# Kernel optimization log

Measured on AMD Instinct MI355X. Metric: run time of the kernel, lower is better.

The kernel has to match this reference:

```python
import jax, jax.numpy as jnp
import numpy as np

K = 3  # hardcoded in TransitionUp.forward

def setup_inputs() -> dict:
    key = jax.random.key(0)
    ks = jax.random.split(key, 8)
    M, N = 32768, 8192
    UP_C, DOWN_C, OUT_C = 128, 256, 128
    return {
        "up_points": jax.random.normal(ks[0], (M, 3), dtype=jnp.float32),
        "up_features": jax.random.normal(ks[1], (M, UP_C), dtype=jnp.float32),
        "down_points": jax.random.normal(ks[2], (N, 3), dtype=jnp.float32),
        "down_features": jax.random.normal(ks[3], (N, DOWN_C), dtype=jnp.float32),
        # torch nn.Linear params: W [out,in], b [out]
        "W_up": jax.random.normal(ks[4], (OUT_C, UP_C), dtype=jnp.float32) / np.sqrt(UP_C),
        "b_up": jax.random.normal(ks[5], (OUT_C,), dtype=jnp.float32) * 0.01,
        "W_down": jax.random.normal(ks[6], (OUT_C, DOWN_C), dtype=jnp.float32) / np.sqrt(DOWN_C),
        "b_down": jax.random.normal(ks[7], (OUT_C,), dtype=jnp.float32) * 0.01,
    }

def interpolate_knn(query_points, dataset_points, dataset_features, k):
    # squared pairwise distances [M, N]
    delta = query_points[:, None, :] - dataset_points[None, :, :]
    dist = jnp.sum(delta * delta, axis=-1)
    neg_dist, knn_idx = jax.lax.top_k(-dist, k)  # smallest-k
    knn_dist = -neg_dist                           # [M, k]
    knn_feats = dataset_features[knn_idx]          # [M, k, C]
    recip = 1.0 / (knn_dist + 1e-8)
    weights = recip / jnp.sum(recip, axis=-1, keepdims=True)  # [M, k]
    return jnp.einsum('mk,mkc->mc', weights, knn_feats)

def reference(up_points, up_features, down_points, down_features, W_up, b_up, W_down, b_down):
    down_f = down_features @ W_down.T + b_down            # [N, OUT_C]
    interp_f = interpolate_knn(up_points, down_points, down_f, K)  # [M, OUT_C]
    return interp_f + (up_features @ W_up.T + b_up)
```

## Files before the change

### kernel.cpp

```cpp
#include <hip/hip_runtime.h>
#include <cfloat>

#define M_UP   32768
#define N_DOWN 8192
#define UPC    128
#define DOWNC  256
#define OUTC   128
#define NCHUNK 8
#define CHUNK  (N_DOWN / NCHUNK)
#define G      8
#define Q      2
#define PG     12

__device__ __forceinline__ void fma4(float4& acc, float s, const float4 w) {
    acc.x = fmaf(s, w.x, acc.x);
    acc.y = fmaf(s, w.y, acc.y);
    acc.z = fmaf(s, w.z, acc.z);
    acc.w = fmaf(s, w.w, acc.w);
}

__device__ __forceinline__ void top3_bl(float s, int idx,
                                        float& d0, float& d1, float& d2,
                                        int& i0, int& i1, int& i2) {
    bool c0 = s < d0, c1 = s < d1, c2 = s < d2;
    float n0 = fminf(d0, s);
    float n1 = __builtin_amdgcn_fmed3f(d0, d1, s);
    float n2 = __builtin_amdgcn_fmed3f(d1, d2, s);
    int m0 = c0 ? idx : i0;
    int m1 = c0 ? i0 : (c1 ? idx : i1);
    int m2 = c1 ? i1 : (c2 ? idx : i2);
    d0 = n0; d1 = n1; d2 = n2;
    i0 = m0; i1 = m1; i2 = m2;
}

__global__ __launch_bounds__(256) void transpose_w(
        const float* __restrict__ W_up, const float* __restrict__ W_down,
        float* __restrict__ wt_up, float* __restrict__ wt_down) {
    int e = blockIdx.x * 256 + threadIdx.x;
    if (e < DOWNC * OUTC) {
        int k = e >> 7, c = e & 127;
        wt_down[e] = W_down[c * DOWNC + k];
    } else {
        int e2 = e - DOWNC * OUTC;
        int k = e2 >> 7, c = e2 & 127;
        wt_up[e2] = W_up[c * UPC + k];
    }
}

template <int K>
__device__ __forceinline__ void gemm_tile32(
        const float* __restrict__ A, const float* __restrict__ WT,
        float* sA , float* sW ,
        int rbase, int tid, float4 acc[2][2]) {
    const int rl = tid & 15;
    const int c0 = (tid >> 4) * 8;
    #pragma unroll 1
    for (int ph = 0; ph < K / 32; ++ph) {
        if (ph) __syncthreads();
        {
            int r = tid >> 3, k4 = tid & 7;
            float4 v = *(const float4*)(A + (size_t)(rbase + r) * K + ph * 32 + k4 * 4);
            *(float4*)&sA[r * 36 + k4 * 4] = v;
        }
        #pragma unroll
        for (int i = 0; i < 4; ++i) {
            int idx = tid + i * 256;
            int kk = idx >> 5, cc = idx & 31;
            float4 v = *(const float4*)(WT + (size_t)(ph * 32 + kk) * OUTC + cc * 4);
            *(float4*)&sW[kk * OUTC + cc * 4] = v;
        }
        __syncthreads();
        #pragma unroll 4
        for (int kk = 0; kk < 32; ++kk) {
            float a0 = sA[rl * 36 + kk];
            float a1 = sA[(rl + 16) * 36 + kk];
            float4 w0 = *(const float4*)&sW[kk * OUTC + c0];
            float4 w1 = *(const float4*)&sW[kk * OUTC + c0 + 4];
            fma4(acc[0][0], a0, w0); fma4(acc[0][1], a0, w1);
            fma4(acc[1][0], a1, w0); fma4(acc[1][1], a1, w1);
        }
    }
}

__device__ __forceinline__ void down_body(
        const float* __restrict__ A, const float* __restrict__ WT,
        const float* __restrict__ bias, float* __restrict__ down_f,
        int rb, int tid, float* smem) {
    float* sA = smem;
    float* sW = smem + 1152;
    float4 acc[2][2] = {};
    gemm_tile32<DOWNC>(A, WT, sA, sW, rb * 32, tid, acc);
    const int rl = tid & 15;
    const int cg = (tid >> 4) * 2;
    const float4 b0 = ((const float4*)bias)[cg];
    const float4 b1 = ((const float4*)bias)[cg + 1];
    #pragma unroll
    for (int i = 0; i < 2; ++i) {
        const int row = rb * 32 + rl + 16 * i;
        float4 v0 = acc[i][0], v1 = acc[i][1];
        v0.x += b0.x; v0.y += b0.y; v0.z += b0.z; v0.w += b0.w;
        v1.x += b1.x; v1.y += b1.y; v1.z += b1.z; v1.w += b1.w;
        ((float4*)down_f)[row * 32 + cg] = v0;
        ((float4*)down_f)[row * 32 + cg + 1] = v1;
    }
}

__device__ __forceinline__ void knn_body(
        const float* __restrict__ up_points,
        const float* __restrict__ down_points,
        float2* __restrict__ part,
        int bx, int by, int tid, float* smem) {
    float* sx = smem;
    float* sy = smem + 1536;
    float* sz = smem + 3072;
    const int base = by * CHUNK;
    for (int t = tid; t < CHUNK; t += 256) {
        int g = base + t;
        int gi = t >> 3, j = t & 7;
        sx[PG * gi + j] = down_points[3 * g];
        sy[PG * gi + j] = down_points[3 * g + 1];
        sz[PG * gi + j] = down_points[3 * g + 2];
    }
    __syncthreads();

    const int m0 = bx * (256 * Q) + tid;
    const int m1 = m0 + 256;
    const float q0x = up_points[3 * m0];
    const float q0y = up_points[3 * m0 + 1];
    const float q0z = up_points[3 * m0 + 2];
    const float q1x = up_points[3 * m1];
    const float q1y = up_points[3 * m1 + 1];
    const float q1z = up_points[3 * m1 + 2];

    float a_gd0 = FLT_MAX, a_gd1 = FLT_MAX, a_gd2 = FLT_MAX;
    int   a_gi0 = 0, a_gi1 = 0, a_gi2 = 0;
    float b_gd0 = FLT_MAX, b_gd1 = FLT_MAX, b_gd2 = FLT_MAX;
    int   b_gi0 = 0, b_gi1 = 0, b_gi2 = 0;

    for (int gi = 0; gi < CHUNK / G; ++gi) {
        float4 x0 = *(const float4*)&sx[PG * gi], x1 = *(const float4*)&sx[PG * gi + 4];
        float4 y0 = *(const float4*)&sy[PG * gi], y1 = *(const float4*)&sy[PG * gi + 4];
        float4 z0 = *(const float4*)&sz[PG * gi], z1 = *(const float4*)&sz[PG * gi + 4];
        float px[G] = {x0.x, x0.y, x0.z, x0.w, x1.x, x1.y, x1.z, x1.w};
        float py[G] = {y0.x, y0.y, y0.z, y0.w, y1.x, y1.y, y1.z, y1.w};
        float pz[G] = {z0.x, z0.y, z0.z, z0.w, z1.x, z1.y, z1.z, z1.w};
        float s0[G], s1[G];
        #pragma unroll
        for (int j = 0; j < G; ++j) {
            float dx0 = q0x - px[j], dy0 = q0y - py[j], dz0 = q0z - pz[j];
            s0[j] = fmaf(dz0, dz0, fmaf(dy0, dy0, dx0 * dx0));
            float dx1 = q1x - px[j], dy1 = q1y - py[j], dz1 = q1z - pz[j];
            s1[j] = fmaf(dz1, dz1, fmaf(dy1, dy1, dx1 * dx1));
        }
        float gm0 = fminf(fminf(fminf(s0[0], s0[1]), fminf(s0[2], s0[3])),
                          fminf(fminf(s0[4], s0[5]), fminf(s0[6], s0[7])));
        float gm1 = fminf(fminf(fminf(s1[0], s1[1]), fminf(s1[2], s1[3])),
                          fminf(fminf(s1[4], s1[5]), fminf(s1[6], s1[7])));
        top3_bl(gm0, gi, a_gd0, a_gd1, a_gd2, a_gi0, a_gi1, a_gi2);
        top3_bl(gm1, gi, b_gd0, b_gd1, b_gd2, b_gi0, b_gi1, b_gi2);
    }

    #pragma unroll
    for (int qq = 0; qq < Q; ++qq) {
        const float qx = qq ? q1x : q0x;
        const float qy = qq ? q1y : q0y;
        const float qz = qq ? q1z : q0z;
        int bases[3];
        if (qq == 0) { bases[0] = a_gi0; bases[1] = a_gi1; bases[2] = a_gi2; }
        else         { bases[0] = b_gi0; bases[1] = b_gi1; bases[2] = b_gi2; }
        float D0 = FLT_MAX, D1 = FLT_MAX, D2 = FLT_MAX;
        int I0 = 0, I1 = 0, I2 = 0;
        #pragma unroll
        for (int t = 0; t < 3; ++t) {
            const int gb = bases[t];
            float4 x0 = *(const float4*)&sx[PG * gb], x1 = *(const float4*)&sx[PG * gb + 4];
            float4 y0 = *(const float4*)&sy[PG * gb], y1 = *(const float4*)&sy[PG * gb + 4];
            float4 z0 = *(const float4*)&sz[PG * gb], z1 = *(const float4*)&sz[PG * gb + 4];
            float px[G] = {x0.x, x0.y, x0.z, x0.w, x1.x, x1.y, x1.z, x1.w};
            float py[G] = {y0.x, y0.y, y0.z, y0.w, y1.x, y1.y, y1.z, y1.w};
            float pz[G] = {z0.x, z0.y, z0.z, z0.w, z1.x, z1.y, z1.z, z1.w};
            #pragma unroll
            for (int j = 0; j < G; ++j) {
                float dx = qx - px[j], dy = qy - py[j], dz = qz - pz[j];
                float s = fmaf(dz, dz, fmaf(dy, dy, dx * dx));
                top3_bl(s, base + gb * G + j, D0, D1, D2, I0, I1, I2);
            }
        }
        const int m = qq ? m1 : m0;
        const int o = (by * M_UP + m) * 3;
        part[o]     = make_float2(D0, __int_as_float(I0));
        part[o + 1] = make_float2(D1, __int_as_float(I1));
        part[o + 2] = make_float2(D2, __int_as_float(I2));
    }
}

__device__ __forceinline__ void upg_body(
        const float* __restrict__ A, const float* __restrict__ WT,
        const float* __restrict__ bias, float* __restrict__ out,
        int rb, int tid, float* smem) {
    float* sAT = smem;
    float* sW  = smem + 2304;
    const int rt4 = (tid >> 4) * 4;
    const int ct  = tid & 15;
    const int rbase = rb * 64;

    float4 acc[4][2] = {};
    #pragma unroll 1
    for (int ph = 0; ph < UPC / 32; ++ph) {
        if (ph) __syncthreads();
        {
            const int r = tid & 63, kq = tid >> 6;
            const float* Ar = A + (size_t)(rbase + r) * UPC + ph * 32 + kq * 8;
            float4 v0 = *(const float4*)Ar;
            float4 v1 = *(const float4*)(Ar + 4);
            const int k0 = kq * 8;
            sAT[(k0 + 0) * 72 + r] = v0.x; sAT[(k0 + 1) * 72 + r] = v0.y;
            sAT[(k0 + 2) * 72 + r] = v0.z; sAT[(k0 + 3) * 72 + r] = v0.w;
            sAT[(k0 + 4) * 72 + r] = v1.x; sAT[(k0 + 5) * 72 + r] = v1.y;
            sAT[(k0 + 6) * 72 + r] = v1.z; sAT[(k0 + 7) * 72 + r] = v1.w;
        }
        {
            const float4* Wp = (const float4*)(WT + (size_t)ph * 32 * OUTC);
            float4* sW4 = (float4*)sW;
            #pragma unroll
            for (int i = 0; i < 4; ++i)
                sW4[tid + i * 256] = Wp[tid + i * 256];
        }
        __syncthreads();
        #pragma unroll 4
        for (int kk = 0; kk < 32; ++kk) {
            float4 a  = *(const float4*)&sAT[kk * 72 + rt4];
            float4 w0 = *(const float4*)&sW[kk * 128 + ct * 4];
            float4 w1 = *(const float4*)&sW[kk * 128 + 64 + ct * 4];
            fma4(acc[0][0], a.x, w0); fma4(acc[0][1], a.x, w1);
            fma4(acc[1][0], a.y, w0); fma4(acc[1][1], a.y, w1);
            fma4(acc[2][0], a.z, w0); fma4(acc[2][1], a.z, w1);
            fma4(acc[3][0], a.w, w0); fma4(acc[3][1], a.w, w1);
        }
    }
    const float4 b0 = ((const float4*)bias)[ct];
    const float4 b1 = ((const float4*)bias)[ct + 16];
    float4* out4 = (float4*)out;
    #pragma unroll
    for (int i = 0; i < 4; ++i) {
        const int m = rbase + rt4 + i;
        float4 v0 = acc[i][0], v1 = acc[i][1];
        v0.x += b0.x; v0.y += b0.y; v0.z += b0.z; v0.w += b0.w;
        v1.x += b1.x; v1.y += b1.y; v1.z += b1.z; v1.w += b1.w;
        out4[m * 32 + ct] = v0;
        out4[m * 32 + ct + 16] = v1;
    }
}

__global__ __launch_bounds__(256) void fused_dp_knn(
        const float* __restrict__ down_features, const float* __restrict__ wt_down,
        const float* __restrict__ b_down, float* __restrict__ down_f,
        const float* __restrict__ up_points, const float* __restrict__ down_points,
        float2* __restrict__ part,
        const float* __restrict__ up_features, const float* __restrict__ wt_up,
        const float* __restrict__ b_up, float* __restrict__ out) {
    __shared__ __align__(16) float smem[6400];
    const int bid = blockIdx.x;
    const int grp = bid / 5, rid = bid % 5;
    if (rid < 2) {
        const int kidx = grp * 2 + rid;
        knn_body(up_points, down_points, part, kidx & 63, kidx >> 6,
                 threadIdx.x, smem);
    } else if (rid == 2) {
        down_body(down_features, wt_down, b_down, down_f, grp,
                  threadIdx.x, smem);
    } else {
        const int uidx = grp * 2 + (rid - 3);
        upg_body(up_features, wt_up, b_up, out, uidx, threadIdx.x, smem);
    }
}

__global__ __launch_bounds__(256) void merge_out(
        const float* __restrict__ down_f, const float2* __restrict__ part,
        float* __restrict__ out) {
    __shared__ __align__(16) float2 sPart[NCHUNK][48];
    const int mb = blockIdx.x * 16;
    for (int t = threadIdx.x; t < NCHUNK * 48; t += 256) {
        int s = t / 48, j = t - s * 48;
        sPart[s][j] = part[((size_t)s * M_UP + mb) * 3 + j];
    }
    __syncthreads();

    const int c4 = threadIdx.x & 31;
    const int rr = threadIdx.x >> 5;
    const float4* df4 = (const float4*)down_f;
    float4* out4 = (float4*)out;
    #pragma unroll
    for (int t = 0; t < 2; ++t) {
        const int lr = rr + 8 * t;
        const int m = mb + lr;
        float D0 = FLT_MAX, D1 = FLT_MAX, D2 = FLT_MAX;
        int I0 = 0, I1 = 0, I2 = 0;
        #pragma unroll
        for (int s = 0; s < NCHUNK; ++s) {
            float2 v0 = sPart[s][lr * 3];
            float2 v1 = sPart[s][lr * 3 + 1];
            float2 v2 = sPart[s][lr * 3 + 2];
            top3_bl(v0.x, __float_as_int(v0.y), D0, D1, D2, I0, I1, I2);
            top3_bl(v1.x, __float_as_int(v1.y), D0, D1, D2, I0, I1, I2);
            top3_bl(v2.x, __float_as_int(v2.y), D0, D1, D2, I0, I1, I2);
        }
        float r0 = 1.f / (D0 + 1e-8f);
        float r1 = 1.f / (D1 + 1e-8f);
        float r2 = 1.f / (D2 + 1e-8f);
        float rs = (r0 + r1) + r2;
        float w0 = r0 / rs, w1 = r1 / rs, w2 = r2 / rs;
        float4 f0 = df4[I0 * 32 + c4];
        float4 f1 = df4[I1 * 32 + c4];
        float4 f2 = df4[I2 * 32 + c4];
        float4 o = out4[m * 32 + c4];
        o.x += fmaf(w0, f0.x, fmaf(w1, f1.x, w2 * f2.x));
        o.y += fmaf(w0, f0.y, fmaf(w1, f1.y, w2 * f2.y));
        o.z += fmaf(w0, f0.z, fmaf(w1, f1.z, w2 * f2.z));
        o.w += fmaf(w0, f0.w, fmaf(w1, f1.w, w2 * f2.w));
        out4[m * 32 + c4] = o;
    }
}

extern "C" void kernel_launch(void* const* d_in, const int* in_sizes, int n_in,
                              void* d_out, int out_size, void* d_ws, size_t ws_size,
                              hipStream_t stream) {
    const float* up_points     = (const float*)d_in[0];
    const float* up_features   = (const float*)d_in[1];
    const float* down_points   = (const float*)d_in[2];
    const float* down_features = (const float*)d_in[3];
    const float* W_up          = (const float*)d_in[4];
    const float* b_up          = (const float*)d_in[5];
    const float* W_down        = (const float*)d_in[6];
    const float* b_down        = (const float*)d_in[7];
    float* out = (float*)d_out;

    float* wt_down = (float*)d_ws;
    float* wt_up   = wt_down + DOWNC * OUTC;
    float* down_f  = wt_up + UPC * OUTC;
    float2* part   = (float2*)(down_f + N_DOWN * OUTC);

    transpose_w<<<(DOWNC * OUTC + UPC * OUTC) / 256, 256, 0, stream>>>(
        W_up, W_down, wt_up, wt_down);
    fused_dp_knn<<<1280, 256, 0, stream>>>(
        down_features, wt_down, b_down, down_f, up_points, down_points, part,
        up_features, wt_up, b_up, out);
    merge_out<<<M_UP / 16, 256, 0, stream>>>(down_f, part, out);
}
```

Before: 197.0 us.

## Rebalance fused kernel block roles and widen merge to 64 rows per block

The fused kernel drops the interleaved 5-way role mapping. It now uses 512 dedicated kNN blocks plus 256 blocks that each run one down-projection tile followed by two up-projection tiles, for 768 blocks instead of 1280. The merge kernel now handles 64 query rows per block, with each thread doing 4 rows by 8 columns, so there are fewer blocks and more work per thread. The risks are load imbalance, since the GEMM blocks are now heavier, and less overlap between the kNN and GEMM work.

Measured after the change: 173.3 us. 1.14x faster.

```diff
diff --git a/kernel.cpp b/kernel.cpp
--- a/kernel.cpp
+++ b/kernel.cpp
@@ -171,8 +171,8 @@
         float D0 = FLT_MAX, D1 = FLT_MAX, D2 = FLT_MAX;
         int I0 = 0, I1 = 0, I2 = 0;
         #pragma unroll
-        for (int t = 0; t < 3; ++t) {
-            const int gb = bases[t];
+        for (int t3 = 0; t3 < 3; ++t3) {
+            const int gb = bases[t3];
             float4 x0 = *(const float4*)&sx[PG * gb], x1 = *(const float4*)&sx[PG * gb + 4];
             float4 y0 = *(const float4*)&sy[PG * gb], y1 = *(const float4*)&sy[PG * gb + 4];
             float4 z0 = *(const float4*)&sz[PG * gb], z1 = *(const float4*)&sz[PG * gb + 4];
@@ -261,46 +261,50 @@
         const float* __restrict__ b_up, float* __restrict__ out) {
     __shared__ __align__(16) float smem[6400];
     const int bid = blockIdx.x;
-    const int grp = bid / 5, rid = bid % 5;
-    if (rid < 2) {
-        const int kidx = grp * 2 + rid;
-        knn_body(up_points, down_points, part, kidx & 63, kidx >> 6,
+    if (bid < 512) {
+        knn_body(up_points, down_points, part, bid & 63, bid >> 6,
                  threadIdx.x, smem);
-    } else if (rid == 2) {
-        down_body(down_features, wt_down, b_down, down_f, grp,
+    } else {
+        const int db = bid - 512;
+        down_body(down_features, wt_down, b_down, down_f, db,
                   threadIdx.x, smem);
-    } else {
-        const int uidx = grp * 2 + (rid - 3);
-        upg_body(up_features, wt_up, b_up, out, uidx, threadIdx.x, smem);
-    }
-}
-
-__global__ __launch_bounds__(256) void merge_out(
+        __syncthreads();
+        upg_body(up_features, wt_up, b_up, out, 2 * db, threadIdx.x, smem);
+        __syncthreads();
+        upg_body(up_features, wt_up, b_up, out, 2 * db + 1, threadIdx.x, smem);
+    }
+}
+
+__global__ __launch_bounds__(256) void merge_out64(
         const float* __restrict__ down_f, const float2* __restrict__ part,
         float* __restrict__ out) {
-    __shared__ __align__(16) float2 sPart[NCHUNK][48];
-    const int mb = blockIdx.x * 16;
-    for (int t = threadIdx.x; t < NCHUNK * 48; t += 256) {
-        int s = t / 48, j = t - s * 48;
-        sPart[s][j] = part[((size_t)s * M_UP + mb) * 3 + j];
+    __shared__ __align__(16) float2 sP[NCHUNK * 192];
+    const int tid = threadIdx.x;
+    const int rbase = blockIdx.x * 64;
+    #pragma unroll
+    for (int i = 0; i < 6; ++i) {
+        int t = tid + i * 256;
+        int s = t / 192;
+        int o = t - s * 192;
+        sP[t] = part[((size_t)s * M_UP + rbase) * 3 + o];
     }
     __syncthreads();
 
-    const int c4 = threadIdx.x & 31;
-    const int rr = threadIdx.x >> 5;
+    const int rt4 = (tid >> 4) * 4;
+    const int ct  = tid & 15;
     const float4* df4 = (const float4*)down_f;
     float4* out4 = (float4*)out;
     #pragma unroll
-    for (int t = 0; t < 2; ++t) {
-        const int lr = rr + 8 * t;
-        const int m = mb + lr;
+    for (int i = 0; i < 4; ++i) {
+        const int lr = rt4 + i;
+        const int m = rbase + lr;
         float D0 = FLT_MAX, D1 = FLT_MAX, D2 = FLT_MAX;
         int I0 = 0, I1 = 0, I2 = 0;
         #pragma unroll
         for (int s = 0; s < NCHUNK; ++s) {
-            float2 v0 = sPart[s][lr * 3];
-            float2 v1 = sPart[s][lr * 3 + 1];
-            float2 v2 = sPart[s][lr * 3 + 2];
+            float2 v0 = sP[s * 192 + lr * 3];
+            float2 v1 = sP[s * 192 + lr * 3 + 1];
+            float2 v2 = sP[s * 192 + lr * 3 + 2];
             top3_bl(v0.x, __float_as_int(v0.y), D0, D1, D2, I0, I1, I2);
             top3_bl(v1.x, __float_as_int(v1.y), D0, D1, D2, I0, I1, I2);
             top3_bl(v2.x, __float_as_int(v2.y), D0, D1, D2, I0, I1, I2);
@@ -310,15 +314,21 @@
         float r2 = 1.f / (D2 + 1e-8f);
         float rs = (r0 + r1) + r2;
         float w0 = r0 / rs, w1 = r1 / rs, w2 = r2 / rs;
-        float4 f0 = df4[I0 * 32 + c4];
-        float4 f1 = df4[I1 * 32 + c4];
-        float4 f2 = df4[I2 * 32 + c4];
-        float4 o = out4[m * 32 + c4];
-        o.x += fmaf(w0, f0.x, fmaf(w1, f1.x, w2 * f2.x));
-        o.y += fmaf(w0, f0.y, fmaf(w1, f1.y, w2 * f2.y));
-        o.z += fmaf(w0, f0.z, fmaf(w1, f1.z, w2 * f2.z));
-        o.w += fmaf(w0, f0.w, fmaf(w1, f1.w, w2 * f2.w));
-        out4[m * 32 + c4] = o;
+        float4 f00 = df4[I0 * 32 + ct], f01 = df4[I0 * 32 + ct + 16];
+        float4 f10 = df4[I1 * 32 + ct], f11 = df4[I1 * 32 + ct + 16];
+        float4 f20 = df4[I2 * 32 + ct], f21 = df4[I2 * 32 + ct + 16];
+        float4 o0 = out4[m * 32 + ct];
+        float4 o1 = out4[m * 32 + ct + 16];
+        o0.x += fmaf(w0, f00.x, fmaf(w1, f10.x, w2 * f20.x));
+        o0.y += fmaf(w0, f00.y, fmaf(w1, f10.y, w2 * f20.y));
+        o0.z += fmaf(w0, f00.z, fmaf(w1, f10.z, w2 * f20.z));
+        o0.w += fmaf(w0, f00.w, fmaf(w1, f10.w, w2 * f20.w));
+        o1.x += fmaf(w0, f01.x, fmaf(w1, f11.x, w2 * f21.x));
+        o1.y += fmaf(w0, f01.y, fmaf(w1, f11.y, w2 * f21.y));
+        o1.z += fmaf(w0, f01.z, fmaf(w1, f11.z, w2 * f21.z));
+        o1.w += fmaf(w0, f01.w, fmaf(w1, f11.w, w2 * f21.w));
+        out4[m * 32 + ct] = o0;
+        out4[m * 32 + ct + 16] = o1;
     }
 }
 
@@ -342,8 +352,8 @@
 
     transpose_w<<<(DOWNC * OUTC + UPC * OUTC) / 256, 256, 0, stream>>>(
         W_up, W_down, wt_up, wt_down);
-    fused_dp_knn<<<1280, 256, 0, stream>>>(
+    fused_dp_knn<<<768, 256, 0, stream>>>(
         down_features, wt_down, b_down, down_f, up_points, down_points, part,
         up_features, wt_up, b_up, out);
-    merge_out<<<M_UP / 16, 256, 0, stream>>>(down_f, part, out);
-}
+    merge_out64<<<M_UP / 64, 256, 0, stream>>>(down_f, part, out);
+}
```
